# Optimization experiments

Measured on AMD Instinct MI355X. Metric: run time of the kernel, lower is better.

Reference implementation:

```python
import jax, jax.numpy as jnp
import numpy as np

# MANO kinematic tree (16 LBS joints): wrist root, 5 fingers x 3 joints
PARENTS = np.array([-1, 0, 1, 2, 0, 4, 5, 0, 7, 8, 0, 10, 11, 0, 13, 14])
B, NV, NJ_LBS, NJ_REG, NCOMPS = 4096, 1084, 16, 21, 45


def rodrigues(r):
    """Axis-angle [N,3] -> rotation matrices [N,3,3]."""
    eps = 1e-8
    angle = jnp.sqrt(jnp.sum(r * r, axis=-1, keepdims=True) + eps)  # [N,1]
    axis = r / angle
    c = jnp.cos(angle)[..., None]  # [N,1,1]
    s = jnp.sin(angle)[..., None]
    x, y, z = axis[:, 0], axis[:, 1], axis[:, 2]
    zeros = jnp.zeros_like(x)
    K = jnp.stack([zeros, -z, y, z, zeros, -x, -y, x, zeros], axis=-1).reshape(-1, 3, 3)
    I = jnp.eye(3, dtype=r.dtype)
    return I + s * K + (1.0 - c) * jnp.matmul(K, K)


def global_rigid_transform(Rs, Js):
    """Rs [B,16,3,3], Js [B,16,3] -> (posed joints [B,16,3], relative transforms A [B,16,4,4])."""
    b = Rs.shape[0]
    bottom = jnp.broadcast_to(jnp.array([0.0, 0.0, 0.0, 1.0], dtype=Rs.dtype), (b, 1, 4))

    def make_A(R, t):  # R [B,3,3], t [B,3] -> [B,4,4]
        top = jnp.concatenate([R, t[..., None]], axis=-1)
        return jnp.concatenate([top, bottom], axis=1)

    results = [make_A(Rs[:, 0], Js[:, 0])]
    for i in range(1, NJ_LBS):  # fixed small loop over kinematic tree
        p = int(PARENTS[i])
        t = Js[:, i] - Js[:, p]
        results.append(jnp.matmul(results[p], make_A(Rs[:, i], t)))
    A_world = jnp.stack(results, axis=1)  # [B,16,4,4]
    new_J = A_world[:, :, :3, 3]
    # A = A_world - pack(A_world @ [J;0])  (remove rest-pose joint translation)
    Jh = jnp.concatenate([Js, jnp.zeros_like(Js[..., :1])], axis=-1)  # [B,16,4]
    init_bone = jnp.einsum('bjpq,bjq->bjp', A_world, Jh)  # [B,16,4]
    A_rel = A_world.at[:, :, :, 3].add(-init_bone)
    return new_J, A_rel


def setup_inputs() -> dict:
    key = jax.random.key(0)
    ks = jax.random.split(key, 8)
    beta = jax.random.normal(ks[0], (B, 10), dtype=jnp.float32)
    theta = jax.random.normal(ks[1], (B, NCOMPS), dtype=jnp.float32)
    wrist_euler = jax.random.normal(ks[2], (B, 3), dtype=jnp.float32) * 0.3
    v_template = jax.random.normal(ks[3], (NV, 3), dtype=jnp.float32) * 0.1
    J_regressor = jax.nn.softmax(jax.random.normal(ks[4], (NV, NJ_REG), dtype=jnp.float32) * 4.0, axis=0)
    hands_comp = jax.random.normal(ks[5], (NCOMPS, 45), dtype=jnp.float32) * 0.05
    hands_mean = jax.random.normal(ks[6], (45,), dtype=jnp.float32) * 0.1
    weights = jax.nn.softmax(jax.random.normal(ks[7], (NV, NJ_LBS), dtype=jnp.float32) * 4.0, axis=1)
    return {"beta": beta, "theta": theta, "wrist_euler": wrist_euler,
            "v_template": v_template, "J_regressor": J_regressor,
            "hands_comp": hands_comp, "hands_mean": hands_mean, "weights": weights}


def reference(beta, theta, wrist_euler, v_template, J_regressor, hands_comp, hands_mean, weights):
    num_batch = beta.shape[0]  # beta only sets batch; forward ignores its values (as in source)
    # rest-pose joints from template: [21,3]
    Jt = jnp.einsum('vc,vj->jc', v_template, J_regressor)
    J = jnp.broadcast_to(Jt[None], (num_batch, NJ_REG, 3))
    # pose_type == 'pca'
    euler_pose = theta @ hands_comp + hands_mean  # [B,45]
    Rs = rodrigues(euler_pose.reshape(-1, 3)).reshape(num_batch, 15, 3, 3)
    global_rot = rodrigues(wrist_euler.reshape(-1, 3)).reshape(num_batch, 1, 3, 3)
    R_all = jnp.concatenate([global_rot, Rs], axis=1)  # [B,16,3,3]
    J_transformed, A = global_rigid_transform(R_all, J[:, :NJ_LBS])
    # linear blend skinning: T = W @ A  -> [B,Nv,4,4]
    W = jnp.broadcast_to(weights[None], (num_batch, NV, NJ_LBS))
    T = jnp.matmul(W, A.reshape(num_batch, NJ_LBS, 16)).reshape(num_batch, NV, 4, 4)
    vh = jnp.concatenate([v_template, jnp.ones_like(v_template[:, :1])], axis=-1)  # [Nv,4]
    verts = jnp.einsum('bvpq,vq->bvp', T, vh)[:, :, :3]  # [B,Nv,3]
    joints = jnp.einsum('bvc,vj->bjc', verts, J_regressor)  # [B,21,3]
    return verts, joints
```

## Files before the change

### kernel.cpp

```cpp
#include <hip/hip_runtime.h>

#define NV 1084
#define NVPAD 1088
#define SCW 1088

typedef __attribute__((ext_vector_type(8))) short short8v;
typedef __attribute__((ext_vector_type(4))) float f32x4;

__device__ inline unsigned short f2bf(float f) {
    unsigned int u = __float_as_uint(f);
    unsigned int r = (u + 0x7FFFu + ((u >> 16) & 1u)) >> 16;
    return (unsigned short)r;
}
__device__ inline float bf2f(unsigned short h) {
    unsigned int u = ((unsigned int)h) << 16;
    return __uint_as_float(u);
}


__device__ inline void rodrigues9(float x, float y, float z, float R[9]) {
    float n2 = x * x + y * y + z * z + 1e-8f;
    float angle = sqrtf(n2);
    float inv = 1.0f / angle;
    float ax = x * inv, ay = y * inv, az = z * inv;
    float c = __cosf(angle), s = __sinf(angle);
    float C = 1.0f - c;
    R[0] = 1.0f - C * (ay * ay + az * az);
    R[1] = -s * az + C * ax * ay;
    R[2] = s * ay + C * ax * az;
    R[3] = s * az + C * ax * ay;
    R[4] = 1.0f - C * (ax * ax + az * az);
    R[5] = -s * ax + C * ay * az;
    R[6] = -s * ay + C * ax * az;
    R[7] = s * ax + C * ay * az;
    R[8] = 1.0f - C * (ax * ax + ay * ay);
}

__global__ __launch_bounds__(256) void prep_kernel(
    const float* __restrict__ theta, const float* __restrict__ hc,
    const float* __restrict__ hm, const float* __restrict__ vt,
    const float* __restrict__ jreg, const float* __restrict__ wts,
    float* __restrict__ euler_ws, float* __restrict__ Mfinal,
    unsigned short* __restrict__ Gbf, int B, int nE) {
    int blk = blockIdx.x;
    int t = threadIdx.x;
    if (blk < nE) {
        int i = blk * 256 + t;
        if (i < B * 45) {
            int b = i / 45, col = i - b * 45;
            const float* th = theta + (size_t)b * 45;
            float acc = hm[col];
#pragma unroll
            for (int k = 0; k < 45; ++k) acc += th[k] * hc[k * 45 + col];
            euler_ws[i] = acc;
        }
    } else if (blk < nE + 336) {
        __shared__ float sm[256];
        int m = blk - nE;
        int qi = t >> 6, u = t & 63;
        int q = m * 4 + qi;
        int j = q >> 6, k = (q >> 2) & 15, d = q & 3;
        int v0 = u * 17, v1 = min(v0 + 17, NV);
        float acc = 0.f;
        for (int v = v0; v < v1; ++v) {
            float vh = (d == 3) ? 1.f : vt[v * 3 + d];
            acc += jreg[v * 21 + j] * wts[v * 16 + k] * vh;
        }
        sm[t] = acc;
        __syncthreads();
#pragma unroll
        for (int s = 32; s > 0; s >>= 1) {
            if (u < s) sm[t] += sm[t + s];
            __syncthreads();
        }
        if (u == 0) Mfinal[q] = sm[t];
    } else {
        int idx = (blk - nE - 336) * 256 + t;
        if (idx < NVPAD * 64) {
            int v = idx >> 6, i = idx & 63;
            int k = i >> 2, d = i & 3;
            float val = 0.f;
            if (v < NV) {
                float vh = (d == 3) ? 1.f : vt[v * 3 + d];
                val = wts[v * 16 + k] * vh;
            }
            Gbf[idx] = f2bf(val);
        }
    }
}

__global__ __launch_bounds__(256) void verts_kernel(
    const float* __restrict__ wrist, const float* __restrict__ euler_ws,
    const float* __restrict__ Mfinal, const unsigned short* __restrict__ Gbf,
    float* __restrict__ verts, float* __restrict__ jout) {
    __shared__ float sC[12 * SCW];
    __shared__ unsigned short sAb[16 * 64];
    __shared__ float sj[48];

    int t = threadIdx.x;
    int b0 = blockIdx.x * 4;
    int w = t >> 6, lane = t & 63;
    int lrow = lane & 15, lk = lane >> 4;

    if (t < 48) {
        int j = t / 3, c = t - 3 * (t / 3);
        float acc = 0.f;
#pragma unroll
        for (int k = 0; k < 16; ++k) acc += Mfinal[j * 64 + k * 4 + c];
        sj[t] = acc;
    }
    sAb[768 + t] = 0;
    __syncthreads();

    if (t < 20) {
        int bl = t / 5, r = t - 5 * bl;
        int b = b0 + bl;
        float e[9];
#pragma unroll
        for (int col = 0; col < 9; ++col)
            e[col] = euler_ws[(size_t)b * 45 + 9 * r + col];

        float R[9];
        rodrigues9(wrist[b * 3 + 0], wrist[b * 3 + 1], wrist[b * 3 + 2], R);
        float J0x = sj[0], J0y = sj[1], J0z = sj[2];
        float Ap[12];
        Ap[0] = R[0]; Ap[1] = R[1]; Ap[2] = R[2]; Ap[3] = J0x;
        Ap[4] = R[3]; Ap[5] = R[4]; Ap[6] = R[5]; Ap[7] = J0y;
        Ap[8] = R[6]; Ap[9] = R[7]; Ap[10] = R[8]; Ap[11] = J0z;
        if (r == 0) {
#pragma unroll
            for (int row = 0; row < 3; ++row) {
                float a0 = Ap[row * 4 + 0], a1 = Ap[row * 4 + 1], a2 = Ap[row * 4 + 2];
                float a3 = Ap[row * 4 + 3] - (a0 * J0x + a1 * J0y + a2 * J0z);
                unsigned short* dst = &sAb[(bl * 3 + row) * 64];
                dst[0] = f2bf(a0); dst[1] = f2bf(a1);
                dst[2] = f2bf(a2); dst[3] = f2bf(a3);
            }
        }
        float px = J0x, py = J0y, pz = J0z;
#pragma unroll
        for (int s = 0; s < 3; ++s) {
            int i = r * 3 + s + 1;
            rodrigues9(e[3 * s + 0], e[3 * s + 1], e[3 * s + 2], R);
            float jx = sj[i * 3 + 0], jy = sj[i * 3 + 1], jz = sj[i * 3 + 2];
            float tx = jx - px, ty = jy - py, tz = jz - pz;
            float An[12];
#pragma unroll
            for (int row = 0; row < 3; ++row) {
                An[row * 4 + 0] = Ap[row * 4 + 0] * R[0] + Ap[row * 4 + 1] * R[3] + Ap[row * 4 + 2] * R[6];
                An[row * 4 + 1] = Ap[row * 4 + 0] * R[1] + Ap[row * 4 + 1] * R[4] + Ap[row * 4 + 2] * R[7];
                An[row * 4 + 2] = Ap[row * 4 + 0] * R[2] + Ap[row * 4 + 1] * R[5] + Ap[row * 4 + 2] * R[8];
                An[row * 4 + 3] = Ap[row * 4 + 3] + Ap[row * 4 + 0] * tx + Ap[row * 4 + 1] * ty + Ap[row * 4 + 2] * tz;
            }
#pragma unroll
            for (int row = 0; row < 3; ++row) {
                float a0 = An[row * 4 + 0], a1 = An[row * 4 + 1], a2 = An[row * 4 + 2];
                float a3 = An[row * 4 + 3] - (a0 * jx + a1 * jy + a2 * jz);
                unsigned short* dst = &sAb[(bl * 3 + row) * 64 + 4 * i];
                dst[0] = f2bf(a0); dst[1] = f2bf(a1);
                dst[2] = f2bf(a2); dst[3] = f2bf(a3);
            }
#pragma unroll
            for (int q = 0; q < 12; ++q) Ap[q] = An[q];
            px = jx; py = jy; pz = jz;
        }
    }
    __syncthreads();

    short8v a0 = *(const short8v*)&sAb[lrow * 64 + lk * 8];
    short8v a1 = *(const short8v*)&sAb[lrow * 64 + lk * 8 + 32];
    for (int vt4 = w; vt4 < NVPAD / 16; vt4 += 4) {
        int v = vt4 * 16 + lrow;
        const unsigned short* Br = Gbf + (size_t)v * 64 + lk * 8;
        short8v g0 = *(const short8v*)Br;
        short8v g1 = *(const short8v*)(Br + 32);
        f32x4 acc = {0.f, 0.f, 0.f, 0.f};
        acc = __builtin_amdgcn_mfma_f32_16x16x32_bf16(a0, g0, acc, 0, 0, 0);
        acc = __builtin_amdgcn_mfma_f32_16x16x32_bf16(a1, g1, acc, 0, 0, 0);
        if (lk < 3) {
            float* dst = &sC[(lk * 4) * SCW + vt4 * 16 + lrow];
#pragma unroll
            for (int q = 0; q < 4; ++q) dst[q * SCW] = acc[q];
        }
    }
    __syncthreads();

    float* outp = verts + (size_t)b0 * (NV * 3);
#pragma unroll 1
    for (int f = t; f < 3252; f += 256) {
        int bl = f / 813;
        int off = (f - bl * 813) * 4;
        f32x4 val;
#pragma unroll
        for (int j = 0; j < 4; ++j) {
            int o = off + j;
            int v_ = o / 3, p_ = o - v_ * 3;
            val[j] = sC[(bl * 3 + p_) * SCW + v_];
        }
        __builtin_nontemporal_store(val, (f32x4*)(outp + (size_t)f * 4));
    }

    if (t < 252) {
        int bl = t / 63;
        int rem = t - bl * 63;
        int j = rem / 3;
        int c = rem - j * 3;
        const unsigned short* Ar = &sAb[(bl * 3 + c) * 64];
        const float* Mj = Mfinal + j * 64;
        float acc = 0.f;
#pragma unroll
        for (int k = 0; k < 16; ++k) {
            float4 m = *(const float4*)&Mj[k * 4];
            acc += bf2f(Ar[k * 4 + 0]) * m.x + bf2f(Ar[k * 4 + 1]) * m.y +
                   bf2f(Ar[k * 4 + 2]) * m.z + bf2f(Ar[k * 4 + 3]) * m.w;
        }
        __builtin_nontemporal_store(acc, jout + (size_t)(b0 + bl) * 63 + rem);
    }
}

extern "C" void kernel_launch(void* const* d_in, const int* in_sizes, int n_in,
                              void* d_out, int out_size, void* d_ws, size_t ws_size,
                              hipStream_t stream) {
    const float* theta = (const float*)d_in[1];
    const float* wrist = (const float*)d_in[2];
    const float* vtpl  = (const float*)d_in[3];
    const float* jreg  = (const float*)d_in[4];
    const float* hc    = (const float*)d_in[5];
    const float* hm    = (const float*)d_in[6];
    const float* wts   = (const float*)d_in[7];
    int B = in_sizes[1] / 45;

    float* euler_ws = (float*)d_ws;
    float* Mfinal   = euler_ws + (size_t)B * 45;
    unsigned short* Gbf = (unsigned short*)(Mfinal + 1344);
    float* verts  = (float*)d_out;
    float* jout   = verts + (size_t)B * NV * 3;

    int nE = (B * 45 + 255) / 256;
    prep_kernel<<<nE + 336 + 272, 256, 0, stream>>>(
        theta, hc, hm, vtpl, jreg, wts, euler_ws, Mfinal, Gbf, B, nE);
    verts_kernel<<<B / 4, 256, 0, stream>>>(
        wrist, euler_ws, Mfinal, Gbf, verts, jout);
}
```

Measured before the change: 48.07 us.

## Fuse PCA pose into verts kernel and store vertices directly from MFMA

The PCA pose projection (theta @ hands_comp + hands_mean) moves out of the prep kernel and into the per-batch threads of the verts kernel. This removes the workspace write and read of the euler angles. The 52KB shared-memory staging buffer for output transposition is dropped, and each lane instead scatters its MFMA results straight to global memory with strided scalar stores. This should raise occupancy and remove a barrier plus an LDS pass. The costs are less coalesced output writes and a serial 45x9 dot product on 20 threads per block.

```diff
diff --git a/kernel.cpp b/kernel.cpp
--- a/kernel.cpp
+++ b/kernel.cpp
@@ -2,7 +2,6 @@
 
 #define NV 1084
 #define NVPAD 1088
-#define SCW 1088
 
 typedef __attribute__((ext_vector_type(8))) short short8v;
 typedef __attribute__((ext_vector_type(4))) float f32x4;
@@ -37,28 +36,15 @@
 }
 
 __global__ __launch_bounds__(256) void prep_kernel(
-    const float* __restrict__ theta, const float* __restrict__ hc,
-    const float* __restrict__ hm, const float* __restrict__ vt,
-    const float* __restrict__ jreg, const float* __restrict__ wts,
-    float* __restrict__ euler_ws, float* __restrict__ Mfinal,
-    unsigned short* __restrict__ Gbf, int B, int nE) {
+    const float* __restrict__ vt, const float* __restrict__ jreg,
+    const float* __restrict__ wts, float* __restrict__ Mfinal,
+    unsigned short* __restrict__ Gbf) {
     int blk = blockIdx.x;
     int t = threadIdx.x;
-    if (blk < nE) {
-        int i = blk * 256 + t;
-        if (i < B * 45) {
-            int b = i / 45, col = i - b * 45;
-            const float* th = theta + (size_t)b * 45;
-            float acc = hm[col];
-#pragma unroll
-            for (int k = 0; k < 45; ++k) acc += th[k] * hc[k * 45 + col];
-            euler_ws[i] = acc;
-        }
-    } else if (blk < nE + 336) {
+    if (blk < 336) {
         __shared__ float sm[256];
-        int m = blk - nE;
         int qi = t >> 6, u = t & 63;
-        int q = m * 4 + qi;
+        int q = blk * 4 + qi;
         int j = q >> 6, k = (q >> 2) & 15, d = q & 3;
         int v0 = u * 17, v1 = min(v0 + 17, NV);
         float acc = 0.f;
@@ -75,7 +61,7 @@
         }
         if (u == 0) Mfinal[q] = sm[t];
     } else {
-        int idx = (blk - nE - 336) * 256 + t;
+        int idx = (blk - 336) * 256 + t;
         if (idx < NVPAD * 64) {
             int v = idx >> 6, i = idx & 63;
             int k = i >> 2, d = i & 3;
@@ -90,10 +76,11 @@
 }
 
 __global__ __launch_bounds__(256) void verts_kernel(
-    const float* __restrict__ wrist, const float* __restrict__ euler_ws,
-    const float* __restrict__ Mfinal, const unsigned short* __restrict__ Gbf,
+    const float* __restrict__ theta, const float* __restrict__ wrist,
+    const float* __restrict__ hc, const float* __restrict__ hm,
+    const float* __restrict__ euler_unused, const float* __restrict__ Mfinal,
+    const unsigned short* __restrict__ Gbf,
     float* __restrict__ verts, float* __restrict__ jout) {
-    __shared__ float sC[12 * SCW];
     __shared__ unsigned short sAb[16 * 64];
     __shared__ float sj[48];
 
@@ -116,9 +103,18 @@
         int bl = t / 5, r = t - 5 * bl;
         int b = b0 + bl;
         float e[9];
-#pragma unroll
-        for (int col = 0; col < 9; ++col)
-            e[col] = euler_ws[(size_t)b * 45 + 9 * r + col];
+        {
+            const float* th = theta + (size_t)b * 45;
+            int base = 9 * r;
+#pragma unroll
+            for (int col = 0; col < 9; ++col) e[col] = hm[base + col];
+            for (int k = 0; k < 45; ++k) {
+                float tk = th[k];
+                const float* hck = hc + k * 45 + base;
+#pragma unroll
+                for (int col = 0; col < 9; ++col) e[col] += tk * hck[col];
+            }
+        }
 
         float R[9];
         rodrigues9(wrist[b * 3 + 0], wrist[b * 3 + 1], wrist[b * 3 + 2], R);
@@ -169,6 +165,14 @@
 
     short8v a0 = *(const short8v*)&sAb[lrow * 64 + lk * 8];
     short8v a1 = *(const short8v*)&sAb[lrow * 64 + lk * 8 + 32];
+    int base[4];
+#pragma unroll
+    for (int q = 0; q < 4; ++q) {
+        int m = lk * 4 + q;
+        int bq = m / 3, pq = m - 3 * bq;
+        if (bq > 3) bq = 3;
+        base[q] = (b0 + bq) * (NV * 3) + pq;
+    }
     for (int vt4 = w; vt4 < NVPAD / 16; vt4 += 4) {
         int v = vt4 * 16 + lrow;
         const unsigned short* Br = Gbf + (size_t)v * 64 + lk * 8;
@@ -177,27 +181,13 @@
         f32x4 acc = {0.f, 0.f, 0.f, 0.f};
         acc = __builtin_amdgcn_mfma_f32_16x16x32_bf16(a0, g0, acc, 0, 0, 0);
         acc = __builtin_amdgcn_mfma_f32_16x16x32_bf16(a1, g1, acc, 0, 0, 0);
-        if (lk < 3) {
-            float* dst = &sC[(lk * 4) * SCW + vt4 * 16 + lrow];
-#pragma unroll
-            for (int q = 0; q < 4; ++q) dst[q * SCW] = acc[q];
-        }
-    }
-    __syncthreads();
-
-    float* outp = verts + (size_t)b0 * (NV * 3);
-#pragma unroll 1
-    for (int f = t; f < 3252; f += 256) {
-        int bl = f / 813;
-        int off = (f - bl * 813) * 4;
-        f32x4 val;
-#pragma unroll
-        for (int j = 0; j < 4; ++j) {
-            int o = off + j;
-            int v_ = o / 3, p_ = o - v_ * 3;
-            val[j] = sC[(bl * 3 + p_) * SCW + v_];
-        }
-        __builtin_nontemporal_store(val, (f32x4*)(outp + (size_t)f * 4));
+        if (lk < 3 && v < NV) {
+            int vo = v * 3;
+            verts[base[0] + vo] = acc[0];
+            verts[base[1] + vo] = acc[1];
+            verts[base[2] + vo] = acc[2];
+            verts[base[3] + vo] = acc[3];
+        }
     }
 
     if (t < 252) {
@@ -214,7 +204,7 @@
             acc += bf2f(Ar[k * 4 + 0]) * m.x + bf2f(Ar[k * 4 + 1]) * m.y +
                    bf2f(Ar[k * 4 + 2]) * m.z + bf2f(Ar[k * 4 + 3]) * m.w;
         }
-        __builtin_nontemporal_store(acc, jout + (size_t)(b0 + bl) * 63 + rem);
+        jout[(size_t)(b0 + bl) * 63 + rem] = acc;
     }
 }
 
@@ -230,15 +220,12 @@
     const float* wts   = (const float*)d_in[7];
     int B = in_sizes[1] / 45;
 
-    float* euler_ws = (float*)d_ws;
-    float* Mfinal   = euler_ws + (size_t)B * 45;
+    float* Mfinal = (float*)d_ws;
     unsigned short* Gbf = (unsigned short*)(Mfinal + 1344);
     float* verts  = (float*)d_out;
     float* jout   = verts + (size_t)B * NV * 3;
 
-    int nE = (B * 45 + 255) / 256;
-    prep_kernel<<<nE + 336 + 272, 256, 0, stream>>>(
-        theta, hc, hm, vtpl, jreg, wts, euler_ws, Mfinal, Gbf, B, nE);
+    prep_kernel<<<336 + 272, 256, 0, stream>>>(vtpl, jreg, wts, Mfinal, Gbf);
     verts_kernel<<<B / 4, 256, 0, stream>>>(
-        wrist, euler_ws, Mfinal, Gbf, verts, jout);
-}
+        theta, wrist, hc, hm, nullptr, Mfinal, Gbf, verts, jout);
+}
```

Result: slower. 51.81 us (+7.8%).
